# Kernel tuning notes

Hardware: AMD Instinct MI355X
Metric: run time of the kernel (lower is better)

## Reference

```python
import jax, jax.numpy as jnp
import numpy as np

B, S, H = 4, 8192, 768
NH, HD = 12, 64          # num_heads, head_size
M = 64                   # projection_dim = min(256, HD)
EPS = 1e-6

def setup_inputs() -> dict:
    key = jax.random.key(0)
    ks = jax.random.split(key, 10)
    scale_w = 0.02
    scale_p = 1.0 / np.sqrt(HD)
    return {
        'hidden_states': jax.random.normal(ks[0], (B, S, H), jnp.float32),
        'Wq': jax.random.normal(ks[1], (H, H), jnp.float32) * scale_w,
        'bq': jnp.zeros((H,), jnp.float32),
        'Wk': jax.random.normal(ks[2], (H, H), jnp.float32) * scale_w,
        'bk': jnp.zeros((H,), jnp.float32),
        'Wv': jax.random.normal(ks[3], (H, H), jnp.float32) * scale_w,
        'bv': jnp.zeros((H,), jnp.float32),
        'Wo': jax.random.normal(ks[4], (H, H), jnp.float32) * scale_w,
        'bo': jnp.zeros((H,), jnp.float32),
        'projection_matrix': jax.random.normal(ks[5], (NH, HD, M), jnp.float32) * scale_p,
    }

def reference(hidden_states, Wq, bq, Wk, bk, Wv, bv, Wo, bo, projection_matrix):
    b, s, h = hidden_states.shape
    def heads(x):  # [b,s,h] -> [b,nh,s,hd]
        return x.reshape(b, s, NH, HD).transpose(0, 2, 1, 3)
    q = heads(hidden_states @ Wq + bq)
    k = heads(hidden_states @ Wk + bk)
    v = heads(hidden_states @ Wv + bv)
    # random-feature projection + stabilized exp feature map
    qp = jnp.einsum('bhnd,hdm->bhnm', q, projection_matrix)
    kp = jnp.einsum('bhnd,hdm->bhnm', k, projection_matrix)
    qp = jnp.exp(qp - jnp.max(qp, axis=-1, keepdims=True))
    kp = jnp.exp(kp - jnp.max(kp, axis=-1, keepdims=True))
    # O(n) linear attention: kv summary [b,h,m,hd]
    kv = jnp.einsum('bhnm,bhnd->bhmd', kp, v)
    qkv = jnp.einsum('bhnm,bhmd->bhnd', qp, kv)
    k_sum = jnp.sum(kp, axis=2)                      # [b,h,m]
    normalizer = jnp.einsum('bhnm,bhm->bhn', qp, k_sum)[..., None]
    ctx = qkv / (normalizer + EPS)
    ctx = ctx.transpose(0, 2, 1, 3).reshape(b, s, NH * HD)
    return ctx @ Wo + bo
```

## Files before the change

### kernel.cpp

```cpp
#include <hip/hip_runtime.h>
#include <hip/hip_bf16.h>


#define S_    8192
#define H_    768
#define NH_   12
#define EPS_  1e-6f

typedef unsigned short U16;
typedef short bf16x8 __attribute__((ext_vector_type(8)));
typedef float f32x4  __attribute__((ext_vector_type(4)));

__device__ __forceinline__ U16 f2b(float x) {
  unsigned u = __float_as_uint(x);
  return (U16)((u + 0x7fffu + ((u >> 16) & 1u)) >> 16);
}
__device__ __forceinline__ float b2f(U16 h) {
  return __uint_as_float(((unsigned)h) << 16);
}
__device__ __forceinline__ void gl2lds16(const void* g, void* l) {
  __builtin_amdgcn_global_load_lds(
      (const __attribute__((address_space(1))) void*)g,
      (__attribute__((address_space(3))) void*)l, 16, 0, 0);
}

__global__ void zero_f32(float* __restrict__ p, int n) {
  int i = blockIdx.x * 256 + threadIdx.x;
  if (i < n) p[i] = 0.f;
}

__global__ void cvt_f32_bf16(const float* __restrict__ src, U16* __restrict__ hi, int n4) {
  int i = blockIdx.x * 256 + threadIdx.x;
  if (i >= n4) return;
  float4 x = ((const float4*)src)[i];
  ushort4 h;
  h.x = f2b(x.x); h.y = f2b(x.y); h.z = f2b(x.z); h.w = f2b(x.w);
  ((ushort4*)hi)[i] = h;
}

__global__ void fold_proj(const float* __restrict__ Wq, const float* __restrict__ bq,
                          const float* __restrict__ Wk, const float* __restrict__ bk,
                          const float* __restrict__ P,
                          float* __restrict__ Wqp, float* __restrict__ bqp,
                          float* __restrict__ Wkp, float* __restrict__ bkp) {
  __shared__ float Pl[64 * 64];
  __shared__ float WL[4 * 64];
  int h = blockIdx.y, kc = blockIdx.x, tid = threadIdx.x;
  const float* W  = blockIdx.z ? Wk : Wq;
  const float* bb = blockIdx.z ? bk : bq;
  float* Wout = blockIdx.z ? Wkp : Wqp;
  float* bout = blockIdx.z ? bkp : bqp;
  const float4* P4 = (const float4*)(P + (size_t)h * 4096);
#pragma unroll
  for (int i = 0; i < 4; ++i) ((float4*)Pl)[tid + i * 256] = P4[tid + i * 256];
  WL[tid] = W[(size_t)(kc * 4 + (tid >> 6)) * H_ + h * 64 + (tid & 63)];
  __syncthreads();
  int kl = tid >> 6, m = tid & 63;
  float acc = 0.f;
#pragma unroll
  for (int d = 0; d < 64; ++d) acc += WL[kl * 64 + d] * Pl[d * 64 + m];
  Wout[(size_t)(kc * 4 + kl) * H_ + h * 64 + m] = acc;
  if (kc == 0 && tid < 64) {
    float a2 = 0.f;
    for (int d = 0; d < 64; ++d) a2 += bb[h * 64 + d] * Pl[d * 64 + tid];
    bout[h * 64 + tid] = a2;
  }
}

__global__ void build_cat(const float* __restrict__ Wqp, const float* __restrict__ Wkp,
                          const float* __restrict__ Wv,  const float* __restrict__ Wo,
                          U16* __restrict__ WcatH, U16* __restrict__ WoTH) {
  int k = blockIdx.x * 256 + threadIdx.x;
  int r = blockIdx.y;
  float v; U16* dh; size_t off;
  if (r < 768)       { v = Wqp[(size_t)k * H_ + r];          off = (size_t)r * H_ + k;          dh = WcatH; }
  else if (r < 1536) { v = Wkp[(size_t)k * H_ + (r - 768)];  off = (size_t)r * H_ + k;          dh = WcatH; }
  else if (r < 2304) { v = Wv [(size_t)k * H_ + (r - 1536)]; off = (size_t)r * H_ + k;          dh = WcatH; }
  else               { v = Wo [(size_t)k * H_ + (r - 2304)]; off = (size_t)(r - 2304) * H_ + k; dh = WoTH; }
  dh[off] = f2b(v);
}

__global__ void build_bias(const float* __restrict__ bqp, const float* __restrict__ bkp,
                           const float* __restrict__ bv, float* __restrict__ biasC) {
  int i = blockIdx.x * 256 + threadIdx.x;
  if (i >= 2304) return;
  biasC[i] = i < 768 ? bqp[i] : (i < 1536 ? bkp[i - 768] : bv[i - 1536]);
}

__global__ __launch_bounds__(512, 2) void gemm_qkv(
    const U16* __restrict__ Ahi, const U16* __restrict__ Bhi,
    const float* __restrict__ bias,
    U16* __restrict__ qp, U16* __restrict__ kpT, U16* __restrict__ vT) {
  __shared__ __align__(16) U16 Us[65536];
  const int tid = threadIdx.x, w = tid >> 6, lane = tid & 63;
  const int quad = lane >> 4, l16 = lane & 15;
  const int id = blockIdx.x;
  const int swz = (id & 7) * 144 + (id >> 3);
  const int mt = swz & 127, nt = swz >> 7;
  const int rowA0 = mt * 256, colB0 = nt * 256;
  const int wm = w >> 2, wn = w & 3;
  const int srow = w * 8 + (lane >> 3);
  const int kch = ((lane & 7) ^ (lane >> 3)) * 8;
  const U16* As = Ahi + (size_t)(rowA0 + srow) * H_ + kch;
  const U16* Bs = Bhi + (size_t)(colB0 + srow) * H_ + kch;
  const unsigned lb = (unsigned)(w * 8) * 64;

  f32x4 acc[8][4] = {};

  auto stage = [&](int kt, int bi) {
    const U16* ap = As + kt * 64;
    const U16* bp = Bs + kt * 64;
    unsigned ub = (unsigned)bi * 32768u + lb;
#pragma unroll
    for (int q = 0; q < 4; ++q) {
      gl2lds16(ap + (size_t)(q * 64) * H_, &Us[ub + q * 4096]);
      gl2lds16(bp + (size_t)(q * 64) * H_, &Us[ub + 16384u + q * 4096]);
    }
  };

  stage(0, 0);
  stage(1, 1);
  for (int t = 0; t < 12; ++t) {
    const unsigned ab = (unsigned)(t & 1) * 32768u;
    if (t < 11) asm volatile("s_waitcnt vmcnt(8)" ::: "memory");
    else        asm volatile("s_waitcnt vmcnt(0)" ::: "memory");
    __builtin_amdgcn_sched_barrier(0);
    __builtin_amdgcn_s_barrier();
    __builtin_amdgcn_sched_barrier(0);
#pragma unroll
    for (int ks = 0; ks < 2; ++ks) {
      const int xo = ks * 4 + quad;
#pragma unroll
      for (int mh = 0; mh < 2; ++mh) {
        bf16x8 ah[4], bh[4];
#pragma unroll
        for (int i = 0; i < 4; ++i) {
          int row = wm * 128 + mh * 64 + i * 16 + l16;
          ah[i] = *(const bf16x8*)&Us[ab + row * 64 + ((xo ^ (l16 & 7)) * 8)];
        }
#pragma unroll
        for (int j = 0; j < 4; ++j) {
          int row = wn * 64 + j * 16 + l16;
          bh[j] = *(const bf16x8*)&Us[ab + 16384u + row * 64 + ((xo ^ (l16 & 7)) * 8)];
        }
        __builtin_amdgcn_s_setprio(1);
#pragma unroll
        for (int j = 0; j < 4; ++j)
#pragma unroll
          for (int i = 0; i < 4; ++i)
            acc[mh * 4 + i][j] = __builtin_amdgcn_mfma_f32_16x16x32_bf16(
                ah[i], bh[j], acc[mh * 4 + i][j], 0, 0, 0);
        __builtin_amdgcn_s_setprio(0);
      }
    }
    __builtin_amdgcn_sched_barrier(0);
    __builtin_amdgcn_s_barrier();
    __builtin_amdgcn_sched_barrier(0);
    if (t + 2 < 12) stage(t + 2, t & 1);
  }

  const int col64 = colB0 + wn * 64;
  float bj[4];
#pragma unroll
  for (int j = 0; j < 4; ++j) bj[j] = bias[col64 + j * 16 + l16];
  if (col64 < 768) {
    const int h = col64 >> 6;
#pragma unroll
    for (int f = 0; f < 8; ++f) {
#pragma unroll
      for (int r = 0; r < 4; ++r) {
        int row = rowA0 + wm * 128 + f * 16 + quad * 4 + r;
        float v0 = acc[f][0][r] + bj[0], v1 = acc[f][1][r] + bj[1];
        float v2 = acc[f][2][r] + bj[2], v3 = acc[f][3][r] + bj[3];
        float mx = fmaxf(fmaxf(v0, v1), fmaxf(v2, v3));
        mx = fmaxf(mx, __shfl_xor(mx, 1));
        mx = fmaxf(mx, __shfl_xor(mx, 2));
        mx = fmaxf(mx, __shfl_xor(mx, 4));
        mx = fmaxf(mx, __shfl_xor(mx, 8));
        int b = row >> 13, s = row & 8191;
        size_t base = ((size_t)(b * NH_ + h) * S_ + s) * 64 + l16;
        qp[base +  0] = f2b(__expf(v0 - mx));
        qp[base + 16] = f2b(__expf(v1 - mx));
        qp[base + 32] = f2b(__expf(v2 - mx));
        qp[base + 48] = f2b(__expf(v3 - mx));
      }
    }
  } else {
    const int isv = col64 >= 1536;
    const int h = (col64 - (isv ? 1536 : 768)) >> 6;
    U16* dstT = isv ? vT : kpT;
#pragma unroll
    for (int f = 0; f < 8; ++f) {
      float er[4][4];
#pragma unroll
      for (int r = 0; r < 4; ++r) {
        float v0 = acc[f][0][r] + bj[0], v1 = acc[f][1][r] + bj[1];
        float v2 = acc[f][2][r] + bj[2], v3 = acc[f][3][r] + bj[3];
        if (!isv) {
          float mx = fmaxf(fmaxf(v0, v1), fmaxf(v2, v3));
          mx = fmaxf(mx, __shfl_xor(mx, 1));
          mx = fmaxf(mx, __shfl_xor(mx, 2));
          mx = fmaxf(mx, __shfl_xor(mx, 4));
          mx = fmaxf(mx, __shfl_xor(mx, 8));
          v0 = __expf(v0 - mx); v1 = __expf(v1 - mx);
          v2 = __expf(v2 - mx); v3 = __expf(v3 - mx);
        }
        er[0][r] = v0; er[1][r] = v1; er[2][r] = v2; er[3][r] = v3;
      }
      int n = rowA0 + wm * 128 + f * 16 + quad * 4;
      int b = n >> 13, s = n & 8191;
      int bh = b * NH_ + h;
#pragma unroll
      for (int j = 0; j < 4; ++j) {
        ushort4 o;
        o.x = f2b(er[j][0]); o.y = f2b(er[j][1]);
        o.z = f2b(er[j][2]); o.w = f2b(er[j][3]);
        *(ushort4*)&dstT[((size_t)bh * 64 + j * 16 + l16) * S_ + s] = o;
      }
    }
  }
}

__global__ __launch_bounds__(256, 4) void kv_accum_mfma(
    const U16* __restrict__ kpT, const U16* __restrict__ vT,
    float* __restrict__ kvT) {
  __shared__ __align__(16) U16 Us[2 * 64 * 64];
  const int tid = threadIdx.x, w = tid >> 6, lane = tid & 63;
  const int quad = lane >> 4, l16 = lane & 15;
  const int bh = blockIdx.y;
  const int n0 = blockIdx.x * 512;
  const U16* srcs[4];
  unsigned ldsoff[4];
#pragma unroll
  for (int t = 0; t < 4; ++t) {
    int c = w * 4 + t, buf = c >> 3;
    int r = (c & 7) * 8 + (lane >> 3);
    const U16* base = buf ? kpT : vT;
    srcs[t] = base + ((size_t)bh * 64 + r) * S_ + n0 + (lane & 7) * 8;
    ldsoff[t] = buf * 4096 + (c & 7) * 512;
  }
  f32x4 acc[4] = {};
  float ks[4] = {0.f, 0.f, 0.f, 0.f};
  for (int nc = 0; nc < 512; nc += 64) {
#pragma unroll
    for (int t = 0; t < 4; ++t) gl2lds16(srcs[t] + nc, &Us[ldsoff[t]]);
    __syncthreads();
#pragma unroll
    for (int k0 = 0; k0 < 64; k0 += 32) {
      bf16x8 av = *(const bf16x8*)&Us[(w * 16 + l16) * 64 + k0 + quad * 8];
#pragma unroll
      for (int j = 0; j < 4; ++j) {
        bf16x8 bk = *(const bf16x8*)&Us[4096 + (j * 16 + l16) * 64 + k0 + quad * 8];
        if (w == 0) {
#pragma unroll
          for (int e = 0; e < 8; ++e) ks[j] += b2f((U16)bk[e]);
        }
        acc[j] = __builtin_amdgcn_mfma_f32_16x16x32_bf16(av, bk, acc[j], 0, 0, 0);
      }
    }
    __syncthreads();
  }
#pragma unroll
  for (int j = 0; j < 4; ++j)
#pragma unroll
    for (int r = 0; r < 4; ++r) {
      int d = w * 16 + quad * 4 + r;
      atomicAdd(&kvT[((size_t)bh * 80 + d) * 64 + j * 16 + l16], acc[j][r]);
    }
  if (w == 0) {
#pragma unroll
    for (int j = 0; j < 4; ++j) {
      ks[j] += __shfl_xor(ks[j], 16);
      ks[j] += __shfl_xor(ks[j], 32);
    }
    if (lane < 16) {
#pragma unroll
      for (int j = 0; j < 4; ++j)
        atomicAdd(&kvT[((size_t)bh * 80 + 64) * 64 + j * 16 + lane], ks[j]);
    }
  }
}

__global__ __launch_bounds__(256) void ctx_gemm_k(
    const U16* __restrict__ qp, const float* __restrict__ kvT,
    U16* __restrict__ ctx) {
  __shared__ __align__(16) U16 As[128 * 64];
  __shared__ __align__(16) U16 Bs[80 * 64];
  int bh = blockIdx.y, row0 = blockIdx.x * 128;
  int tid = threadIdx.x, w = tid >> 6, lane = tid & 63;
  int quad = lane >> 4, l16 = lane & 15;
  const U16* Ab = qp + ((size_t)bh * S_ + row0) * 64;
#pragma unroll
  for (int t = 0; t < 4; ++t) {
    int cb = (w * 4 + t) * 64;
    gl2lds16(Ab + (size_t)(cb + lane) * 8, &As[cb * 8]);
  }
  const float4* kv4 = (const float4*)(kvT + (size_t)bh * 5120);
#pragma unroll
  for (int t = 0; t < 5; ++t) {
    int idx = t * 256 + tid;
    float4 f = kv4[idx];
    ushort4 o;
    o.x = f2b(f.x); o.y = f2b(f.y); o.z = f2b(f.z); o.w = f2b(f.w);
    *(ushort4*)&Bs[idx * 4] = o;
  }
  __syncthreads();
  f32x4 acc[2][5] = {};
#pragma unroll
  for (int k0 = 0; k0 < 64; k0 += 32) {
    bf16x8 a[2], fb[5];
#pragma unroll
    for (int i = 0; i < 2; ++i)
      a[i] = *(const bf16x8*)&As[(w * 32 + i * 16 + l16) * 64 + k0 + quad * 8];
#pragma unroll
    for (int j = 0; j < 5; ++j)
      fb[j] = *(const bf16x8*)&Bs[(j * 16 + l16) * 64 + k0 + quad * 8];
#pragma unroll
    for (int j = 0; j < 5; ++j)
#pragma unroll
      for (int i = 0; i < 2; ++i)
        acc[i][j] = __builtin_amdgcn_mfma_f32_16x16x32_bf16(a[i], fb[j], acc[i][j], 0, 0, 0);
  }
  int b = bh / NH_, h = bh - b * NH_;
#pragma unroll
  for (int i = 0; i < 2; ++i) {
#pragma unroll
    for (int r = 0; r < 4; ++r) {
      int s = row0 + w * 32 + i * 16 + quad * 4 + r;
      float nv = __shfl(acc[i][4][r], lane & 48);
      float inv = 1.f / (nv + EPS_);
      size_t base = ((size_t)b * S_ + s) * H_ + h * 64;
#pragma unroll
      for (int j = 0; j < 4; ++j)
        ctx[base + j * 16 + l16] = f2b(acc[i][j][r] * inv);
    }
  }
}

__global__ __launch_bounds__(512, 2) void gemm_out(
    const U16* __restrict__ Ahi, const U16* __restrict__ Bhi,
    const float* __restrict__ bias, float* __restrict__ C) {
  __shared__ __align__(16) U16 Us[65536];
  const int tid = threadIdx.x, w = tid >> 6, lane = tid & 63;
  const int quad = lane >> 4, l16 = lane & 15;
  const int id = blockIdx.x;
  const int swz = (id & 7) * 48 + (id >> 3);
  const int mt = swz & 127, nt = swz >> 7;
  const int rowA0 = mt * 256, colB0 = nt * 256;
  const int wm = w >> 2, wn = w & 3;
  const int srow = w * 8 + (lane >> 3);
  const int kch = ((lane & 7) ^ (lane >> 3)) * 8;
  const U16* As = Ahi + (size_t)(rowA0 + srow) * H_ + kch;
  const U16* Bs = Bhi + (size_t)(colB0 + srow) * H_ + kch;
  const unsigned lb = (unsigned)(w * 8) * 64;

  f32x4 acc[8][4] = {};

  auto stage = [&](int kt, int bi) {
    const U16* ap = As + kt * 64;
    const U16* bp = Bs + kt * 64;
    unsigned ub = (unsigned)bi * 32768u + lb;
#pragma unroll
    for (int q = 0; q < 4; ++q) {
      gl2lds16(ap + (size_t)(q * 64) * H_, &Us[ub + q * 4096]);
      gl2lds16(bp + (size_t)(q * 64) * H_, &Us[ub + 16384u + q * 4096]);
    }
  };

  stage(0, 0);
  stage(1, 1);
  for (int t = 0; t < 12; ++t) {
    const unsigned ab = (unsigned)(t & 1) * 32768u;
    if (t < 11) asm volatile("s_waitcnt vmcnt(8)" ::: "memory");
    else        asm volatile("s_waitcnt vmcnt(0)" ::: "memory");
    __builtin_amdgcn_sched_barrier(0);
    __builtin_amdgcn_s_barrier();
    __builtin_amdgcn_sched_barrier(0);
#pragma unroll
    for (int ks = 0; ks < 2; ++ks) {
      const int xo = ks * 4 + quad;
#pragma unroll
      for (int mh = 0; mh < 2; ++mh) {
        bf16x8 ah[4], bh[4];
#pragma unroll
        for (int i = 0; i < 4; ++i) {
          int row = wm * 128 + mh * 64 + i * 16 + l16;
          ah[i] = *(const bf16x8*)&Us[ab + row * 64 + ((xo ^ (l16 & 7)) * 8)];
        }
#pragma unroll
        for (int j = 0; j < 4; ++j) {
          int row = wn * 64 + j * 16 + l16;
          bh[j] = *(const bf16x8*)&Us[ab + 16384u + row * 64 + ((xo ^ (l16 & 7)) * 8)];
        }
        __builtin_amdgcn_s_setprio(1);
#pragma unroll
        for (int j = 0; j < 4; ++j)
#pragma unroll
          for (int i = 0; i < 4; ++i)
            acc[mh * 4 + i][j] = __builtin_amdgcn_mfma_f32_16x16x32_bf16(
                ah[i], bh[j], acc[mh * 4 + i][j], 0, 0, 0);
        __builtin_amdgcn_s_setprio(0);
      }
    }
    __builtin_amdgcn_sched_barrier(0);
    __builtin_amdgcn_s_barrier();
    __builtin_amdgcn_sched_barrier(0);
    if (t + 2 < 12) stage(t + 2, t & 1);
  }

#pragma unroll
  for (int f = 0; f < 8; ++f) {
    int row = rowA0 + wm * 128 + f * 16 + quad * 4;
#pragma unroll
    for (int j = 0; j < 4; ++j) {
      int col = colB0 + wn * 64 + j * 16 + l16;
      float bvv = bias[col];
#pragma unroll
      for (int r = 0; r < 4; ++r)
        C[(size_t)(row + r) * H_ + col] = acc[f][j][r] + bvv;
    }
  }
}

extern "C" void kernel_launch(void* const* d_in, const int* in_sizes, int n_in,
                              void* d_out, int out_size, void* d_ws, size_t ws_size,
                              hipStream_t stream) {
  const float* hs = (const float*)d_in[0];
  const float* Wq = (const float*)d_in[1];
  const float* bq = (const float*)d_in[2];
  const float* Wk = (const float*)d_in[3];
  const float* bk = (const float*)d_in[4];
  const float* Wv = (const float*)d_in[5];
  const float* bv = (const float*)d_in[6];
  const float* Wo = (const float*)d_in[7];
  const float* bo = (const float*)d_in[8];
  const float* P  = (const float*)d_in[9];
  float* out = (float*)d_out;

  char* ws = (char*)d_ws;
  size_t off = 0;
  auto alloc = [&](size_t bytes) -> void* {
    void* p = ws + off;
    off = (off + bytes + 255) & ~(size_t)255;
    return p;
  };
  U16*   hs_hi = (U16*)alloc(50331648);
  float* WqpF  = (float*)alloc(2359296);
  float* WkpF  = (float*)alloc(2359296);
  float* bqpF  = (float*)alloc(3072);
  float* bkpF  = (float*)alloc(3072);
  U16*   WcatH = (U16*)alloc(3538944);
  U16*   WoTH  = (U16*)alloc(1179648);
  float* biasC = (float*)alloc(9216);
  U16*   qp    = (U16*)alloc(50331648);
  U16*   kpT   = (U16*)alloc(50331648);
  U16*   vT    = (U16*)alloc(50331648);
  float* kvT   = (float*)alloc(983040);
  U16*   ctx   = hs_hi;

  zero_f32<<<dim3(960), dim3(256), 0, stream>>>(kvT, 245760);
  cvt_f32_bf16<<<dim3(24576), dim3(256), 0, stream>>>(hs, hs_hi, 6291456);
  fold_proj<<<dim3(192, 12, 2), dim3(256), 0, stream>>>(Wq, bq, Wk, bk, P, WqpF, bqpF, WkpF, bkpF);
  build_cat<<<dim3(3, 3072), dim3(256), 0, stream>>>(WqpF, WkpF, Wv, Wo, WcatH, WoTH);
  build_bias<<<dim3(9), dim3(256), 0, stream>>>(bqpF, bkpF, bv, biasC);
  gemm_qkv<<<dim3(1152), dim3(512), 0, stream>>>(hs_hi, WcatH, biasC, qp, kpT, vT);
  kv_accum_mfma<<<dim3(16, 48), dim3(256), 0, stream>>>(kpT, vT, kvT);
  ctx_gemm_k<<<dim3(64, 48), dim3(256), 0, stream>>>(qp, kvT, ctx);
  gemm_out<<<dim3(384), dim3(512), 0, stream>>>(ctx, WoTH, bo, out);
}
```

Baseline: 506.0 us.

## Restructure GEMM k-loop into four barrier-synced MFMA phases and remap tiles per XCD

Both GEMMs now share a k-loop macro that issues the next stage's global-to-LDS load at the top of each iteration, so only one tile is in flight instead of two. Each 64-wide k tile is split into four phases, each loading a quarter of the A/B fragments and running its MFMAs between workgroup barriers. The block-to-tile mapping also changes so each XCD owns a contiguous band of M tiles and walks every N tile for them, aiming at better L2 reuse of A rows. The extra barriers and shallower prefetch can expose more load latency in exchange for a tighter LDS-read/MFMA interleave.

```diff
diff --git a/kernel.cpp b/kernel.cpp
--- a/kernel.cpp
+++ b/kernel.cpp
@@ -87,6 +87,92 @@
   biasC[i] = i < 768 ? bqp[i] : (i < 1536 ? bkp[i - 768] : bv[i - 1536]);
 }
 
+#define GEMM_KLOOP()                                                         \
+  auto stage = [&](int kt, int bi) {                                         \
+    const U16* ap = As + kt * 64;                                            \
+    const U16* bp = Bs + kt * 64;                                            \
+    unsigned ub = (unsigned)bi * 32768u + lb;                                \
+    _Pragma("unroll")                                                        \
+    for (int q = 0; q < 4; ++q) {                                            \
+      gl2lds16(ap + (size_t)(q * 64) * H_, &Us[ub + q * 4096]);              \
+      gl2lds16(bp + (size_t)(q * 64) * H_, &Us[ub + 16384u + q * 4096]);     \
+    }                                                                        \
+  };                                                                         \
+  auto swzo = [&](int ks) { return (((ks * 4 + quad) ^ (l16 & 7)) * 8); };   \
+  stage(0, 0);                                                               \
+  for (int t = 0; t < 12; ++t) {                                             \
+    const unsigned ab = (unsigned)(t & 1) * 32768u;                          \
+    if (t < 11) {                                                            \
+      stage(t + 1, (t + 1) & 1);                                             \
+      asm volatile("s_waitcnt vmcnt(8)" ::: "memory");                       \
+    } else {                                                                 \
+      asm volatile("s_waitcnt vmcnt(0)" ::: "memory");                       \
+    }                                                                        \
+    __builtin_amdgcn_sched_barrier(0);                                       \
+    __builtin_amdgcn_s_barrier();                                            \
+    __builtin_amdgcn_sched_barrier(0);                                       \
+    bf16x8 ah[8], bh[4];                                                     \
+                              \
+    _Pragma("unroll")                                                        \
+    for (int i = 0; i < 4; ++i)                                              \
+      _Pragma("unroll")                                                      \
+      for (int ks = 0; ks < 2; ++ks)                                         \
+        ah[i * 2 + ks] = *(const bf16x8*)&Us[ab +                            \
+            (unsigned)((wm * 128 + i * 16 + l16) * 64 + swzo(ks))];          \
+    _Pragma("unroll")                                                        \
+    for (int jj = 0; jj < 2; ++jj)                                           \
+      _Pragma("unroll")                                                      \
+      for (int ks = 0; ks < 2; ++ks)                                         \
+        bh[jj * 2 + ks] = *(const bf16x8*)&Us[ab + 16384u +                  \
+            (unsigned)((wn * 64 + jj * 16 + l16) * 64 + swzo(ks))];          \
+    PHASE_TAIL(0, 0)                                                         \
+                                          \
+    _Pragma("unroll")                                                        \
+    for (int jj = 0; jj < 2; ++jj)                                           \
+      _Pragma("unroll")                                                      \
+      for (int ks = 0; ks < 2; ++ks)                                         \
+        bh[jj * 2 + ks] = *(const bf16x8*)&Us[ab + 16384u +                  \
+            (unsigned)((wn * 64 + (2 + jj) * 16 + l16) * 64 + swzo(ks))];    \
+    PHASE_TAIL(0, 1)                                                         \
+                              \
+    _Pragma("unroll")                                                        \
+    for (int i = 0; i < 4; ++i)                                              \
+      _Pragma("unroll")                                                      \
+      for (int ks = 0; ks < 2; ++ks)                                         \
+        ah[i * 2 + ks] = *(const bf16x8*)&Us[ab +                            \
+            (unsigned)((wm * 128 + 64 + i * 16 + l16) * 64 + swzo(ks))];     \
+    PHASE_TAIL(1, 1)                                                         \
+                              \
+    _Pragma("unroll")                                                        \
+    for (int jj = 0; jj < 2; ++jj)                                           \
+      _Pragma("unroll")                                                      \
+      for (int ks = 0; ks < 2; ++ks)                                         \
+        bh[jj * 2 + ks] = *(const bf16x8*)&Us[ab + 16384u +                  \
+            (unsigned)((wn * 64 + jj * 16 + l16) * 64 + swzo(ks))];          \
+    PHASE_TAIL(1, 0)                                                         \
+  }
+
+#define PHASE_TAIL(mh, jh)                                                   \
+    __builtin_amdgcn_sched_barrier(0);                                       \
+    __builtin_amdgcn_s_barrier();                                            \
+    asm volatile("s_waitcnt lgkmcnt(0)" ::: "memory");                       \
+    __builtin_amdgcn_sched_barrier(0);                                       \
+    __builtin_amdgcn_s_setprio(1);                                           \
+    _Pragma("unroll")                                                        \
+    for (int jj = 0; jj < 2; ++jj)                                           \
+      _Pragma("unroll")                                                      \
+      for (int i = 0; i < 4; ++i)                                            \
+        _Pragma("unroll")                                                    \
+        for (int ks = 0; ks < 2; ++ks)                                       \
+          acc[(mh) * 4 + i][(jh) * 2 + jj] =                                 \
+              __builtin_amdgcn_mfma_f32_16x16x32_bf16(                       \
+                  ah[i * 2 + ks], bh[jj * 2 + ks],                           \
+                  acc[(mh) * 4 + i][(jh) * 2 + jj], 0, 0, 0);                \
+    __builtin_amdgcn_s_setprio(0);                                           \
+    __builtin_amdgcn_sched_barrier(0);                                       \
+    __builtin_amdgcn_s_barrier();                                            \
+    __builtin_amdgcn_sched_barrier(0);
+
 __global__ __launch_bounds__(512, 2) void gemm_qkv(
     const U16* __restrict__ Ahi, const U16* __restrict__ Bhi,
     const float* __restrict__ bias,
@@ -95,8 +181,8 @@
   const int tid = threadIdx.x, w = tid >> 6, lane = tid & 63;
   const int quad = lane >> 4, l16 = lane & 15;
   const int id = blockIdx.x;
-  const int swz = (id & 7) * 144 + (id >> 3);
-  const int mt = swz & 127, nt = swz >> 7;
+  const int xcd = id & 7, pos = id >> 3;
+  const int mt = xcd * 16 + pos / 9, nt = pos % 9;
   const int rowA0 = mt * 256, colB0 = nt * 256;
   const int wm = w >> 2, wn = w & 3;
   const int srow = w * 8 + (lane >> 3);
@@ -106,58 +192,7 @@
   const unsigned lb = (unsigned)(w * 8) * 64;
 
   f32x4 acc[8][4] = {};
-
-  auto stage = [&](int kt, int bi) {
-    const U16* ap = As + kt * 64;
-    const U16* bp = Bs + kt * 64;
-    unsigned ub = (unsigned)bi * 32768u + lb;
-#pragma unroll
-    for (int q = 0; q < 4; ++q) {
-      gl2lds16(ap + (size_t)(q * 64) * H_, &Us[ub + q * 4096]);
-      gl2lds16(bp + (size_t)(q * 64) * H_, &Us[ub + 16384u + q * 4096]);
-    }
-  };
-
-  stage(0, 0);
-  stage(1, 1);
-  for (int t = 0; t < 12; ++t) {
-    const unsigned ab = (unsigned)(t & 1) * 32768u;
-    if (t < 11) asm volatile("s_waitcnt vmcnt(8)" ::: "memory");
-    else        asm volatile("s_waitcnt vmcnt(0)" ::: "memory");
-    __builtin_amdgcn_sched_barrier(0);
-    __builtin_amdgcn_s_barrier();
-    __builtin_amdgcn_sched_barrier(0);
-#pragma unroll
-    for (int ks = 0; ks < 2; ++ks) {
-      const int xo = ks * 4 + quad;
-#pragma unroll
-      for (int mh = 0; mh < 2; ++mh) {
-        bf16x8 ah[4], bh[4];
-#pragma unroll
-        for (int i = 0; i < 4; ++i) {
-          int row = wm * 128 + mh * 64 + i * 16 + l16;
-          ah[i] = *(const bf16x8*)&Us[ab + row * 64 + ((xo ^ (l16 & 7)) * 8)];
-        }
-#pragma unroll
-        for (int j = 0; j < 4; ++j) {
-          int row = wn * 64 + j * 16 + l16;
-          bh[j] = *(const bf16x8*)&Us[ab + 16384u + row * 64 + ((xo ^ (l16 & 7)) * 8)];
-        }
-        __builtin_amdgcn_s_setprio(1);
-#pragma unroll
-        for (int j = 0; j < 4; ++j)
-#pragma unroll
-          for (int i = 0; i < 4; ++i)
-            acc[mh * 4 + i][j] = __builtin_amdgcn_mfma_f32_16x16x32_bf16(
-                ah[i], bh[j], acc[mh * 4 + i][j], 0, 0, 0);
-        __builtin_amdgcn_s_setprio(0);
-      }
-    }
-    __builtin_amdgcn_sched_barrier(0);
-    __builtin_amdgcn_s_barrier();
-    __builtin_amdgcn_sched_barrier(0);
-    if (t + 2 < 12) stage(t + 2, t & 1);
-  }
+  GEMM_KLOOP()
 
   const int col64 = colB0 + wn * 64;
   float bj[4];
@@ -209,13 +244,13 @@
       }
       int n = rowA0 + wm * 128 + f * 16 + quad * 4;
       int b = n >> 13, s = n & 8191;
-      int bh = b * NH_ + h;
+      int bh2 = b * NH_ + h;
 #pragma unroll
       for (int j = 0; j < 4; ++j) {
         ushort4 o;
         o.x = f2b(er[j][0]); o.y = f2b(er[j][1]);
         o.z = f2b(er[j][2]); o.w = f2b(er[j][3]);
-        *(ushort4*)&dstT[((size_t)bh * 64 + j * 16 + l16) * S_ + s] = o;
+        *(ushort4*)&dstT[((size_t)bh2 * 64 + j * 16 + l16) * S_ + s] = o;
       }
     }
   }
@@ -344,8 +379,8 @@
   const int tid = threadIdx.x, w = tid >> 6, lane = tid & 63;
   const int quad = lane >> 4, l16 = lane & 15;
   const int id = blockIdx.x;
-  const int swz = (id & 7) * 48 + (id >> 3);
-  const int mt = swz & 127, nt = swz >> 7;
+  const int xcd = id & 7, pos = id >> 3;
+  const int mt = xcd * 16 + pos / 3, nt = pos % 3;
   const int rowA0 = mt * 256, colB0 = nt * 256;
   const int wm = w >> 2, wn = w & 3;
   const int srow = w * 8 + (lane >> 3);
@@ -355,58 +390,7 @@
   const unsigned lb = (unsigned)(w * 8) * 64;
 
   f32x4 acc[8][4] = {};
-
-  auto stage = [&](int kt, int bi) {
-    const U16* ap = As + kt * 64;
-    const U16* bp = Bs + kt * 64;
-    unsigned ub = (unsigned)bi * 32768u + lb;
-#pragma unroll
-    for (int q = 0; q < 4; ++q) {
-      gl2lds16(ap + (size_t)(q * 64) * H_, &Us[ub + q * 4096]);
-      gl2lds16(bp + (size_t)(q * 64) * H_, &Us[ub + 16384u + q * 4096]);
-    }
-  };
-
-  stage(0, 0);
-  stage(1, 1);
-  for (int t = 0; t < 12; ++t) {
-    const unsigned ab = (unsigned)(t & 1) * 32768u;
-    if (t < 11) asm volatile("s_waitcnt vmcnt(8)" ::: "memory");
-    else        asm volatile("s_waitcnt vmcnt(0)" ::: "memory");
-    __builtin_amdgcn_sched_barrier(0);
-    __builtin_amdgcn_s_barrier();
-    __builtin_amdgcn_sched_barrier(0);
-#pragma unroll
-    for (int ks = 0; ks < 2; ++ks) {
-      const int xo = ks * 4 + quad;
-#pragma unroll
-      for (int mh = 0; mh < 2; ++mh) {
-        bf16x8 ah[4], bh[4];
-#pragma unroll
-        for (int i = 0; i < 4; ++i) {
-          int row = wm * 128 + mh * 64 + i * 16 + l16;
-          ah[i] = *(const bf16x8*)&Us[ab + row * 64 + ((xo ^ (l16 & 7)) * 8)];
-        }
-#pragma unroll
-        for (int j = 0; j < 4; ++j) {
-          int row = wn * 64 + j * 16 + l16;
-          bh[j] = *(const bf16x8*)&Us[ab + 16384u + row * 64 + ((xo ^ (l16 & 7)) * 8)];
-        }
-        __builtin_amdgcn_s_setprio(1);
-#pragma unroll
-        for (int j = 0; j < 4; ++j)
-#pragma unroll
-          for (int i = 0; i < 4; ++i)
-            acc[mh * 4 + i][j] = __builtin_amdgcn_mfma_f32_16x16x32_bf16(
-                ah[i], bh[j], acc[mh * 4 + i][j], 0, 0, 0);
-        __builtin_amdgcn_s_setprio(0);
-      }
-    }
-    __builtin_amdgcn_sched_barrier(0);
-    __builtin_amdgcn_s_barrier();
-    __builtin_amdgcn_sched_barrier(0);
-    if (t + 2 < 12) stage(t + 2, t & 1);
-  }
+  GEMM_KLOOP()
 
 #pragma unroll
   for (int f = 0; f < 8; ++f) {
```

After: 496.2 us. About the same (-1.9%).
